# Performance work log

Measured on AMD Instinct MI355X. Metric: run time of the kernel, lower is better.

The kernel has to match this reference:

```python
import jax, jax.numpy as jnp
import numpy as np

LAM = 0.003  # kernel_lam squash threshold


def setup_inputs() -> dict:
    key = jax.random.key(0)
    k1, k2, k3, k4 = jax.random.split(key, 4)
    B, L, H, Lk = 2, 4096, 2048, 128
    u = jax.random.normal(k1, (B, L, H), jnp.float32)
    # LongConvKernel parameter [channels=1, H, Lk]; scaled so squash keeps most taps nonzero
    kernel = jax.random.normal(k2, (1, H, Lk), jnp.float32) * 0.05
    D = jax.random.normal(k3, (1, H), jnp.float32)  # skip term [channels, H]
    # output_linear: nn.Linear(H, 2H) followed by GLU(dim=-1)
    W = jax.random.normal(k4, (2 * H, H), jnp.float32) / np.sqrt(H)
    b = jnp.zeros((2 * H,), jnp.float32)
    return {"u": u, "kernel": kernel, "D": D, "W": W, "b": b}


def reference(u, kernel, D, W, b):
    # u: [B, L, H] -> transpose to [B, H, L]
    B, L, H = u.shape
    ut = jnp.transpose(u, (0, 2, 1)).astype(jnp.float32)  # bhl
    # LongConvKernel forward: squash k = relu(|k| - lam) * sign(k)
    k = jnp.maximum(jnp.abs(kernel) - LAM, 0.0) * jnp.sign(kernel)  # [C, H, Lk]
    Lk = kernel.shape[-1]
    n = Lk + L  # FFT size for linear (causal) convolution
    k_f = jnp.fft.rfft(k, n=n)          # [C, H, n//2+1]
    u_f = jnp.fft.rfft(ut, n=n)         # [B, H, n//2+1]
    y_f = jnp.einsum('bhl,chl->bchl', u_f, k_f)
    y = jnp.fft.irfft(y_f, n=n)[..., :L]  # [B, C, H, L]
    # source adds the D skip term twice (duplicated line) -> factor 2
    y = y + 2.0 * jnp.einsum('bhl,ch->bchl', ut, D)
    # rearrange 'b c h l -> b (c h) l' then transpose -> [B, L, C*H]
    y = jnp.transpose(y.reshape(B, -1, L), (0, 2, 1))
    y = jax.nn.gelu(y, approximate=False)  # torch GELU is exact erf
    z = y @ W.T + b                     # [B, L, 2H]
    a, g = jnp.split(z, 2, axis=-1)     # GLU along last dim
    return a * jax.nn.sigmoid(g)        # [B, L, H]
```

## Files before the change

### kernel.cpp

```cpp
#include <hip/hip_runtime.h>
#include <hip/hip_bf16.h>
#include <cstdint>

constexpr int Bc  = 2;
constexpr int Lc  = 4096;
constexpr int Hc  = 2048;
constexpr int LKc = 128;
constexpr float LAMc = 0.003f;

typedef __attribute__((ext_vector_type(8))) __bf16 bf16x8;
typedef __attribute__((ext_vector_type(4))) float  f32x4;

__device__ __forceinline__ void gl_lds16(const void* g, void* lds) {
  __builtin_amdgcn_global_load_lds(
      (const __attribute__((address_space(1))) uint32_t*)(uintptr_t)g,
      (__attribute__((address_space(3))) uint32_t*)(uint32_t)(uintptr_t)lds,
      16, 0, 0);
}

__global__ __launch_bounds__(256) void squash_kernel(
    const float* __restrict__ kin, float* __restrict__ kq) {
  const int idx = blockIdx.x * 256 + threadIdx.x;
  const int j = idx >> 11;
  const int h = idx & (Hc - 1);
  const float v = kin[h * LKc + j];
  const float a = fabsf(v) - LAMc;
  kq[idx] = (a > 0.f) ? copysignf(a, v) : 0.f;
}

__global__ __launch_bounds__(256) void wcast_kernel(
    const float* __restrict__ W, __hip_bfloat16* __restrict__ Wb) {
  const int idx = (blockIdx.x * 256 + threadIdx.x) * 4;
  const float4 v = *(const float4*)(W + idx);
  Wb[idx + 0] = __float2bfloat16(v.x);
  Wb[idx + 1] = __float2bfloat16(v.y);
  Wb[idx + 2] = __float2bfloat16(v.z);
  Wb[idx + 3] = __float2bfloat16(v.w);
}

template <bool CHECK>
__device__ __forceinline__ void conv_accum(
    const float* __restrict__ ub, const float* __restrict__ kq,
    const int h, const int l0, float acc[16], float win[23]) {
#pragma unroll
  for (int x = 0; x < 23; ++x) {
    const int il = l0 - 127 + x;
    win[x] = (!CHECK || il >= 0) ? ub[(size_t)il * Hc] : 0.f;
  }
#pragma unroll 4
  for (int c = 0; c < 15; ++c) {
    float t[8];
#pragma unroll
    for (int d = 0; d < 8; ++d) t[d] = kq[(127 - 8 * c - d) * Hc + h];
#pragma unroll
    for (int d = 0; d < 8; ++d)
#pragma unroll
      for (int i = 0; i < 16; ++i)
        acc[i] = fmaf(t[d], win[i + d], acc[i]);
#pragma unroll
    for (int x = 0; x < 15; ++x) win[x] = win[x + 8];
#pragma unroll
    for (int x = 15; x < 23; ++x) {
      const int il = l0 - 127 + 8 * (c + 1) + x;
      win[x] = (!CHECK || il >= 0) ? ub[(size_t)il * Hc] : 0.f;
    }
  }
  {
    float t[8];
#pragma unroll
    for (int d = 0; d < 8; ++d) t[d] = kq[(7 - d) * Hc + h];
#pragma unroll
    for (int d = 0; d < 8; ++d)
#pragma unroll
      for (int i = 0; i < 16; ++i)
        acc[i] = fmaf(t[d], win[i + d], acc[i]);
  }
}

__global__ __launch_bounds__(256) void conv_gelu_kernel(
    const float* __restrict__ u, const float* __restrict__ kq,
    const float* __restrict__ Dp, __hip_bfloat16* __restrict__ Aout) {
  const int lane = threadIdx.x & 63;
  const int wv   = threadIdx.x >> 6;
  const int h  = blockIdx.y * 64 + lane;
  const int l0 = blockIdx.x * 64 + wv * 16;
  const int b  = blockIdx.z;
  const float* ub = u + (size_t)b * Lc * Hc + h;

  float acc[16], win[23];
#pragma unroll
  for (int i = 0; i < 16; ++i) acc[i] = 0.f;

  if (blockIdx.x >= 2)
    conv_accum<false>(ub, kq, h, l0, acc, win);
  else
    conv_accum<true>(ub, kq, h, l0, acc, win);

  const float dv = 2.f * Dp[h];
  const size_t obase = ((size_t)b * Lc + l0) * (size_t)Hc + h;
#pragma unroll
  for (int i = 0; i < 16; ++i) {
    const float y  = fmaf(dv, win[i + 7], acc[i]);
    const float ge = 0.5f * y * (1.f + erff(y * 0.70710678118654752f));
    Aout[obase + (size_t)i * Hc] = __float2bfloat16(ge);
  }
}

__global__ __launch_bounds__(256, 2) void gemm_glu_kernel(
    const __hip_bfloat16* __restrict__ A, const __hip_bfloat16* __restrict__ Wb,
    const float* __restrict__ bias, float* __restrict__ out) {
  __shared__ __align__(16) __hip_bfloat16 As[128 * 32];
  __shared__ __align__(16) __hip_bfloat16 Bs[128 * 32];

  const int t    = threadIdx.x;
  const int lane = t & 63;
  const int wv   = t >> 6;
  const int quad = lane >> 4;
  const int l16  = lane & 15;
  const int m0 = blockIdx.x * 128;
  const int n0 = blockIdx.y * 64;

  f32x4 accA[2][4], accG[2][4];
#pragma unroll
  for (int i = 0; i < 2; ++i)
#pragma unroll
    for (int j = 0; j < 4; ++j) {
      accA[i][j] = f32x4{0.f, 0.f, 0.f, 0.f};
      accG[i][j] = f32x4{0.f, 0.f, 0.f, 0.f};
    }

  const int srow = t >> 2;
  const int scol = (t & 3) * 8;
  const __hip_bfloat16* gA0 = A  + (size_t)(m0 + srow) * Hc + scol;
  const __hip_bfloat16* gA1 = A  + (size_t)(m0 + 64 + srow) * Hc + scol;
  const __hip_bfloat16* gBa = Wb + (size_t)(n0 + srow) * Hc + scol;
  const __hip_bfloat16* gBg = Wb + (size_t)(Hc + n0 + srow) * Hc + scol;
  char* ldsA0 = (char*)As + wv * 1024;
  char* ldsA1 = (char*)As + 4096 + wv * 1024;
  char* ldsBa = (char*)Bs + wv * 1024;
  char* ldsBg = (char*)Bs + 4096 + wv * 1024;

  const bf16x8* ar0 = (const bf16x8*)(As + (wv * 32 + l16) * 32 + quad * 8);
  const bf16x8* ar1 = (const bf16x8*)(As + (wv * 32 + 16 + l16) * 32 + quad * 8);

  for (int it = 0; it < 64; ++it) {
    const int k0 = it * 32;
    gl_lds16(gA0 + k0, ldsA0);
    gl_lds16(gA1 + k0, ldsA1);
    gl_lds16(gBa + k0, ldsBa);
    gl_lds16(gBg + k0, ldsBg);
    __syncthreads();
    const bf16x8 af0 = *ar0;
    const bf16x8 af1 = *ar1;
#pragma unroll
    for (int nj = 0; nj < 4; ++nj) {
      const bf16x8 ba = *(const bf16x8*)(Bs + (nj * 16 + l16) * 32 + quad * 8);
      const bf16x8 bg = *(const bf16x8*)(Bs + (64 + nj * 16 + l16) * 32 + quad * 8);
      accA[0][nj] = __builtin_amdgcn_mfma_f32_16x16x32_bf16(af0, ba, accA[0][nj], 0, 0, 0);
      accA[1][nj] = __builtin_amdgcn_mfma_f32_16x16x32_bf16(af1, ba, accA[1][nj], 0, 0, 0);
      accG[0][nj] = __builtin_amdgcn_mfma_f32_16x16x32_bf16(af0, bg, accG[0][nj], 0, 0, 0);
      accG[1][nj] = __builtin_amdgcn_mfma_f32_16x16x32_bf16(af1, bg, accG[1][nj], 0, 0, 0);
    }
    __syncthreads();
  }

  const int mbase = m0 + wv * 32;
#pragma unroll
  for (int mi = 0; mi < 2; ++mi) {
#pragma unroll
    for (int nj = 0; nj < 4; ++nj) {
      const int n = n0 + nj * 16 + l16;
      const float ba_ = bias[n];
      const float bg_ = bias[Hc + n];
#pragma unroll
      for (int r = 0; r < 4; ++r) {
        const int m = mbase + mi * 16 + quad * 4 + r;
        const float a = accA[mi][nj][r] + ba_;
        const float g = accG[mi][nj][r] + bg_;
        out[(size_t)m * Hc + n] = a * (1.f / (1.f + expf(-g)));
      }
    }
  }
}

extern "C" void kernel_launch(void* const* d_in, const int* in_sizes, int n_in,
                              void* d_out, int out_size, void* d_ws, size_t ws_size,
                              hipStream_t stream) {
  const float* u    = (const float*)d_in[0];
  const float* kin  = (const float*)d_in[1];
  const float* Dp   = (const float*)d_in[2];
  const float* W    = (const float*)d_in[3];
  const float* bias = (const float*)d_in[4];
  float* out = (float*)d_out;

  char* ws = (char*)d_ws;
  float*          kq = (float*)ws;
  __hip_bfloat16* Wb = (__hip_bfloat16*)(ws + (1 << 20));
  __hip_bfloat16* Am = (__hip_bfloat16*)(ws + (17 << 20));

  squash_kernel<<<(Hc * LKc) / 256, 256, 0, stream>>>(kin, kq);
  wcast_kernel<<<(2 * Hc * Hc) / 1024, 256, 0, stream>>>(W, Wb);
  conv_gelu_kernel<<<dim3(Lc / 64, Hc / 64, Bc), 256, 0, stream>>>(u, kq, Dp, Am);
  gemm_glu_kernel<<<dim3((Bc * Lc) / 128, Hc / 64), 256, 0, stream>>>(Am, Wb, bias, out);
}
```

Before: 393.1 us.

## Compute causal long convolution with bf16 MFMA Toeplitz fragments

Replaces the scalar FP32 FMA direct convolution with an MFMA formulation. A precomputed kernel builds per-channel Toeplitz-shaped bf16 tap fragments, and the conv kernel stages a reversed bf16 window of u in LDS before running five 16x16x32 MFMAs per channel tile. The output goes through an LDS transpose so stores are coalesced. This lowers the cost of the conv stage but adds bf16 rounding of u and the taps in the convolution, and the tap-fragment buffer reuses the workspace region later overwritten by the weight cast.

```diff
diff --git a/kernel.cpp b/kernel.cpp
--- a/kernel.cpp
+++ b/kernel.cpp
@@ -10,6 +10,13 @@
 
 typedef __attribute__((ext_vector_type(8))) __bf16 bf16x8;
 typedef __attribute__((ext_vector_type(4))) float  f32x4;
+typedef __attribute__((ext_vector_type(8))) unsigned short ushort8;
+
+__device__ __forceinline__ unsigned short f2bf_bits(float v) {
+  union { __hip_bfloat16 b; unsigned short u; } cv;
+  cv.b = __float2bfloat16(v);
+  return cv.u;
+}
 
 __device__ __forceinline__ void gl_lds16(const void* g, void* lds) {
   __builtin_amdgcn_global_load_lds(
@@ -18,14 +25,28 @@
       16, 0, 0);
 }
 
-__global__ __launch_bounds__(256) void squash_kernel(
-    const float* __restrict__ kin, float* __restrict__ kq) {
-  const int idx = blockIdx.x * 256 + threadIdx.x;
-  const int j = idx >> 11;
-  const int h = idx & (Hc - 1);
-  const float v = kin[h * LKc + j];
-  const float a = fabsf(v) - LAMc;
-  kq[idx] = (a > 0.f) ? copysignf(a, v) : 0.f;
+__global__ __launch_bounds__(256) void tapfrag_kernel(
+    const float* __restrict__ kin, unsigned short* __restrict__ Afr) {
+  const int idx  = blockIdx.x * 256 + threadIdx.x;
+  const int lane = idx & 63;
+  const int idx2 = idx >> 6;
+  const int h  = idx2 / 5;
+  const int cc = idx2 - h * 5;
+  const int m = lane & 15, quad = lane >> 4;
+  const int jb = m + 32 * cc - 32 + 8 * quad;
+  ushort8 o;
+#pragma unroll
+  for (int jj = 0; jj < 8; ++jj) {
+    const int j = jb + jj;
+    float v = 0.f;
+    if (j >= 0 && j < LKc) {
+      const float x = kin[h * LKc + j];
+      const float a = fabsf(x) - LAMc;
+      v = (a > 0.f) ? copysignf(a, x) : 0.f;
+    }
+    o[jj] = f2bf_bits(v);
+  }
+  ((ushort8*)Afr)[idx] = o;
 }
 
 __global__ __launch_bounds__(256) void wcast_kernel(
@@ -38,71 +59,74 @@
   Wb[idx + 3] = __float2bfloat16(v.w);
 }
 
-template <bool CHECK>
-__device__ __forceinline__ void conv_accum(
-    const float* __restrict__ ub, const float* __restrict__ kq,
-    const int h, const int l0, float acc[16], float win[23]) {
-#pragma unroll
-  for (int x = 0; x < 23; ++x) {
-    const int il = l0 - 127 + x;
-    win[x] = (!CHECK || il >= 0) ? ub[(size_t)il * Hc] : 0.f;
-  }
-#pragma unroll 4
-  for (int c = 0; c < 15; ++c) {
-    float t[8];
-#pragma unroll
-    for (int d = 0; d < 8; ++d) t[d] = kq[(127 - 8 * c - d) * Hc + h];
-#pragma unroll
-    for (int d = 0; d < 8; ++d)
-#pragma unroll
-      for (int i = 0; i < 16; ++i)
-        acc[i] = fmaf(t[d], win[i + d], acc[i]);
-#pragma unroll
-    for (int x = 0; x < 15; ++x) win[x] = win[x + 8];
-#pragma unroll
-    for (int x = 15; x < 23; ++x) {
-      const int il = l0 - 127 + 8 * (c + 1) + x;
-      win[x] = (!CHECK || il >= 0) ? ub[(size_t)il * Hc] : 0.f;
-    }
-  }
+__global__ __launch_bounds__(256) void conv_mfma_kernel(
+    const float* __restrict__ u, const unsigned short* __restrict__ Afr,
+    const float* __restrict__ Dp, unsigned short* __restrict__ Am) {
+  __shared__ __align__(16) unsigned short ur[16 * 408];
+  __shared__ __align__(16) float          uc[16 * 260];
+  __shared__ __align__(16) unsigned short ot[256 * 17];
+
+  const int t    = threadIdx.x;
+  const int lane = t & 63;
+  const int wv   = t >> 6;
+  const int l16  = lane & 15;
+  const int quad = lane >> 4;
+  const int l0 = blockIdx.x * 256;
+  const int h0 = blockIdx.y * 16;
+  const int b  = blockIdx.z;
+
+  const size_t ubase = (size_t)b * Lc * Hc + h0;
+
+#pragma unroll
+  for (int i = 0; i < 25; ++i) {
+    const int e  = (i << 8) + t;
+    const int hl = e & 15;
+    const int x  = e >> 4;
+    const int l  = l0 + 272 - x;
+    float v = 0.f;
+    if (l >= 0) v = u[ubase + (size_t)min(l, Lc - 1) * Hc + hl];
+    ur[hl * 408 + x] = f2bf_bits(v);
+    const int lc = l - l0;
+    if (lc >= 0 && lc < 256) uc[hl * 260 + lc] = v;
+  }
+  __syncthreads();
+
+#pragma unroll
+  for (int hi = 0; hi < 4; ++hi) {
+    const int hl = (wv << 2) | hi;
+    const int h  = h0 + hl;
+    f32x4 acc = f32x4{0.f, 0.f, 0.f, 0.f};
+    const unsigned short* afp = Afr + ((size_t)(h * 5) * 64 + lane) * 8;
+    const int bbase = hl * 408 + 240 - 16 * l16 + 8 * quad;
+#pragma unroll
+    for (int cc = 0; cc < 5; ++cc) {
+      const bf16x8 af = *(const bf16x8*)(afp + cc * 512);
+      const bf16x8 bf = *(const bf16x8*)(&ur[bbase + 32 * cc]);
+      acc = __builtin_amdgcn_mfma_f32_16x16x32_bf16(af, bf, acc, 0, 0, 0);
+    }
+    const float dv = 2.f * Dp[h];
+    const float4 u4 = *(const float4*)(&uc[hl * 260 + quad * 4 + 16 * l16]);
+    const float uu[4] = {u4.x, u4.y, u4.z, u4.w};
+#pragma unroll
+    for (int r = 0; r < 4; ++r) {
+      const int lc = quad * 4 + r + 16 * l16;
+      const float y = fmaf(dv, uu[r], acc[r]);
+      const float g = 0.5f * y * (1.f + erff(y * 0.70710678118654752f));
+      ot[lc * 17 + hl] = f2bf_bits(g);
+    }
+  }
+  __syncthreads();
+
   {
-    float t[8];
-#pragma unroll
-    for (int d = 0; d < 8; ++d) t[d] = kq[(7 - d) * Hc + h];
-#pragma unroll
-    for (int d = 0; d < 8; ++d)
-#pragma unroll
-      for (int i = 0; i < 16; ++i)
-        acc[i] = fmaf(t[d], win[i + d], acc[i]);
-  }
-}
-
-__global__ __launch_bounds__(256) void conv_gelu_kernel(
-    const float* __restrict__ u, const float* __restrict__ kq,
-    const float* __restrict__ Dp, __hip_bfloat16* __restrict__ Aout) {
-  const int lane = threadIdx.x & 63;
-  const int wv   = threadIdx.x >> 6;
-  const int h  = blockIdx.y * 64 + lane;
-  const int l0 = blockIdx.x * 64 + wv * 16;
-  const int b  = blockIdx.z;
-  const float* ub = u + (size_t)b * Lc * Hc + h;
-
-  float acc[16], win[23];
-#pragma unroll
-  for (int i = 0; i < 16; ++i) acc[i] = 0.f;
-
-  if (blockIdx.x >= 2)
-    conv_accum<false>(ub, kq, h, l0, acc, win);
-  else
-    conv_accum<true>(ub, kq, h, l0, acc, win);
-
-  const float dv = 2.f * Dp[h];
-  const size_t obase = ((size_t)b * Lc + l0) * (size_t)Hc + h;
-#pragma unroll
-  for (int i = 0; i < 16; ++i) {
-    const float y  = fmaf(dv, win[i + 7], acc[i]);
-    const float ge = 0.5f * y * (1.f + erff(y * 0.70710678118654752f));
-    Aout[obase + (size_t)i * Hc] = __float2bfloat16(ge);
+    const int lc = t;
+    const unsigned short* row = &ot[lc * 17];
+    unsigned int w[8];
+#pragma unroll
+    for (int p = 0; p < 8; ++p)
+      w[p] = (unsigned int)row[2 * p] | ((unsigned int)row[2 * p + 1] << 16);
+    unsigned short* dst = Am + ((size_t)(b * Lc + l0 + lc)) * Hc + h0;
+    *(uint4*)(dst)     = make_uint4(w[0], w[1], w[2], w[3]);
+    *(uint4*)(dst + 8) = make_uint4(w[4], w[5], w[6], w[7]);
   }
 }
 
@@ -194,12 +218,13 @@
   float* out = (float*)d_out;
 
   char* ws = (char*)d_ws;
-  float*          kq = (float*)ws;
-  __hip_bfloat16* Wb = (__hip_bfloat16*)(ws + (1 << 20));
-  __hip_bfloat16* Am = (__hip_bfloat16*)(ws + (17 << 20));
-
-  squash_kernel<<<(Hc * LKc) / 256, 256, 0, stream>>>(kin, kq);
+  unsigned short* Afr = (unsigned short*)ws;
+  __hip_bfloat16* Wb  = (__hip_bfloat16*)ws;
+  unsigned short* Am  = (unsigned short*)(ws + (16 << 20));
+
+  tapfrag_kernel<<<(Hc * 5 * 64) / 256, 256, 0, stream>>>(kin, Afr);
+  conv_mfma_kernel<<<dim3(Lc / 256, Hc / 16, Bc), 256, 0, stream>>>(u, Afr, Dp, Am);
   wcast_kernel<<<(2 * Hc * Hc) / 1024, 256, 0, stream>>>(W, Wb);
-  conv_gelu_kernel<<<dim3(Lc / 64, Hc / 64, Bc), 256, 0, stream>>>(u, kq, Dp, Am);
-  gemm_glu_kernel<<<dim3((Bc * Lc) / 128, Hc / 64), 256, 0, stream>>>(Am, Wb, bias, out);
-}
+  gemm_glu_kernel<<<dim3((Bc * Lc) / 128, Hc / 64), 256, 0, stream>>>(
+      (const __hip_bfloat16*)Am, Wb, bias, out);
+}
```

After: 391.7 us. No clear change (-0.4%).
